# Optimization experiments

Measured on AMD Instinct MI355X. Metric: run time of the kernel, lower is better.

Reference implementation:

```python
import jax, jax.numpy as jnp
import numpy as np

NEG_INF = -1e9  # stands in for the eye(W)*sys.maxsize self-mask on the row axis


def setup_inputs() -> dict:
    key = jax.random.key(0)
    ks = jax.random.split(key, 8)
    B, C, S = 8, 512, 128
    C8 = C // 8
    sc = 0.02
    x = jax.random.normal(ks[0], (B, C, S, S), dtype=jnp.float32)
    Wq = jax.random.normal(ks[1], (C8, C), dtype=jnp.float32) * sc
    bq = jnp.zeros((C8,), dtype=jnp.float32)
    Wk = jax.random.normal(ks[2], (C8, C), dtype=jnp.float32) * sc
    bk = jnp.zeros((C8,), dtype=jnp.float32)
    Wv = jax.random.normal(ks[3], (C, C), dtype=jnp.float32) * sc
    bv = jnp.zeros((C,), dtype=jnp.float32)
    gamma = jnp.ones((1,), dtype=jnp.float32) * 0.5  # source inits to 0; nonzero so path is exercised
    return {"x": x, "Wq": Wq, "bq": bq, "Wk": Wk, "bk": bk, "Wv": Wv, "bv": bv, "gamma": gamma}


def reference(x, Wq, bq, Wk, bk, Wv, bv, gamma):
    # x: (B, C, W, H) with W == H == S (required by the eye-mask view in the source)
    B, C, S, _ = x.shape
    # 1x1 convs = per-pixel linear projections
    q = jnp.einsum('oc,bcwh->bowh', Wq, x) + bq[None, :, None, None]  # (B,C8,S,S)
    k = jnp.einsum('oc,bcwh->bowh', Wk, x) + bk[None, :, None, None]
    v = jnp.einsum('oc,bcwh->bowh', Wv, x) + bv[None, :, None, None]  # (B,C,S,S)

    # column ('h'-fixed) attention along W, self position masked out
    e_col = jnp.einsum('bcwh,bcuh->bwhu', q, k)  # (B,W,H,W)
    self_mask = jnp.eye(S, dtype=bool)  # w == u
    e_col = jnp.where(self_mask[None, :, None, :], NEG_INF, e_col)
    # row ('w'-fixed) attention along H
    e_row = jnp.einsum('bcwh,bcwu->bwhu', q, k)  # (B,W,H,H)

    att = jax.nn.softmax(jnp.concatenate([e_col, e_row], axis=-1), axis=-1)  # (B,W,H,2S)
    a_col = att[..., :S]   # weights over w'
    a_row = att[..., S:]   # weights over h'

    out = (jnp.einsum('bwhu,bcuh->bcwh', a_col, v)
           + jnp.einsum('bwhu,bcwu->bcwh', a_row, v))  # (B,C,S,S)
    return gamma[0] * out + x
```

## Files before the change

kernel.cpp:

```cpp
#include <hip/hip_runtime.h>
#include <hip/hip_bf16.h>


#define S 128
#define SS 16384
#define C 512
#define C8 64
#define NEG_BIG -1000000000.0f

using short8 = __attribute__((ext_vector_type(8))) short;
using f32x4  = __attribute__((ext_vector_type(4))) float;

#define GPTR(p) ((const __attribute__((address_space(1))) void*)(p))
#define LPTR(p) ((__attribute__((address_space(3))) void*)(p))

__device__ __forceinline__ unsigned short f2b(float f){
  union { float f; unsigned u; } v; v.f = f;
  unsigned r = (v.u + 0x7fffu + ((v.u >> 16) & 1u)) >> 16;
  return (unsigned short)r;
}
__device__ __forceinline__ float b2f(unsigned short h){
  union { unsigned u; float f; } v; v.u = ((unsigned)h) << 16;
  return v.f;
}

__global__ __launch_bounds__(256) void k_pack_w(
    const float* __restrict__ Wq, const float* __restrict__ Wk,
    const float* __restrict__ Wv, unsigned short* __restrict__ wall){
  int i = blockIdx.x * 256 + threadIdx.x;
  if (i >= 640 * C) return;
  int co = i >> 9, ci = i & (C - 1);
  float v;
  if (co < 64)        v = Wq[co * C + ci];
  else if (co < 128)  v = Wk[(co - 64) * C + ci];
  else                v = Wv[(co - 128) * C + ci];
  wall[i] = f2b(v);
}

__global__ __launch_bounds__(256) void k_xp(
    const float* __restrict__ x, unsigned short* __restrict__ xp){
  __shared__ unsigned short T[128 * 130] __attribute__((aligned(16)));
  int blk = blockIdx.x;
  int ct = blk & 3; int bw = blk >> 2;
  int w = bw & 127; int b = bw >> 7;
  int tid = threadIdx.x;
  int ci0 = ct * 128;
  const float* xb = x + ((size_t)(b * C + ci0) * S + w) * S;
  #pragma unroll
  for (int p = 0; p < 16; ++p){
    int idx = p * 256 + tid;
    int cc = idx >> 5;
    int h4 = (idx & 31) * 4;
    float4 v = *(const float4*)(xb + (size_t)cc * SS + h4);
    unsigned* d = (unsigned*)&T[cc * 130 + h4];
    d[0] = (unsigned)f2b(v.x) | ((unsigned)f2b(v.y) << 16);
    d[1] = (unsigned)f2b(v.z) | ((unsigned)f2b(v.w) << 16);
  }
  __syncthreads();
  unsigned short* xpb = xp + (size_t)(b * S + w) * S * C + ci0;
  #pragma unroll
  for (int p = 0; p < 8; ++p){
    int idx = p * 256 + tid;
    int h  = idx >> 4;
    int ch = (idx & 15) * 8;
    unsigned short tmp[8] __attribute__((aligned(16)));
    #pragma unroll
    for (int j = 0; j < 8; ++j) tmp[j] = T[(ch + j) * 130 + h];
    *(uint4*)(xpb + (size_t)h * C + ch) = *(uint4*)tmp;
  }
}

__global__ __launch_bounds__(256) void k_qkv(
    const unsigned short* __restrict__ xp, const unsigned short* __restrict__ wall,
    const float* __restrict__ bq, const float* __restrict__ bk,
    const float* __restrict__ bv,
    unsigned short* __restrict__ qp, unsigned short* __restrict__ kp,
    unsigned short* __restrict__ vb){
  __shared__ unsigned short sm[17408] __attribute__((aligned(16)));
  unsigned short* Al = sm;
  unsigned short* Bl = sm + 8192;
  unsigned short* Dl = sm;
  int blk = blockIdx.x;
  int pxsub = blk & 7; int t = blk >> 3;
  int cot = t % 5; int pxg = t / 5;
  int pxt = pxg * 8 + pxsub;
  int w = pxt & 127, b = pxt >> 7;
  int tid = threadIdx.x, lane = tid & 63, wid = tid >> 6;
  int qd = lane >> 4, ln = lane & 15;
  const unsigned short* asrc0 = wall + (size_t)cot * 128 * C;
  const unsigned short* bsrc0 = xp + (size_t)pxt * 128 * C;
  f32x4 acc[4][4];
  #pragma unroll
  for (int i = 0; i < 4; ++i)
    #pragma unroll
    for (int j = 0; j < 4; ++j) acc[i][j] = (f32x4){0.f, 0.f, 0.f, 0.f};

  for (int kw = 0; kw < 8; ++kw){
    __syncthreads();
    const unsigned short* asrc = asrc0 + kw * 64;
    const unsigned short* bsrc = bsrc0 + kw * 64;
    #pragma unroll
    for (int p = 0; p < 4; ++p){
      int gi = p * 256 + tid;
      int row = gi >> 3, kc = (gi & 7) * 8;
      __builtin_amdgcn_global_load_lds(GPTR(asrc + (size_t)row * C + kc),
                                       LPTR((char*)Al + gi * 16), 16, 0, 0);
      __builtin_amdgcn_global_load_lds(GPTR(bsrc + (size_t)row * C + kc),
                                       LPTR((char*)Bl + gi * 16), 16, 0, 0);
    }
    __syncthreads();
    #pragma unroll
    for (int ks = 0; ks < 2; ++ks){
      int ko = ks * 32 + qd * 8;
      short8 af[4], bfr[4];
      #pragma unroll
      for (int i = 0; i < 4; ++i)
        af[i] = *(const short8*)&Al[(((wid & 1) * 4 + i) * 16 + ln) * 64 + ko];
      #pragma unroll
      for (int j = 0; j < 4; ++j)
        bfr[j] = *(const short8*)&Bl[(((wid >> 1) * 4 + j) * 16 + ln) * 64 + ko];
      #pragma unroll
      for (int i = 0; i < 4; ++i)
        #pragma unroll
        for (int j = 0; j < 4; ++j)
          acc[i][j] = __builtin_amdgcn_mfma_f32_16x16x32_bf16(af[i], bfr[j], acc[i][j], 0, 0, 0);
    }
  }
  __syncthreads();
  float bias_[4][4];
  #pragma unroll
  for (int i = 0; i < 4; ++i){
    int co_l0 = ((wid & 1) * 4 + i) * 16 + qd * 4;
    #pragma unroll
    for (int r = 0; r < 4; ++r){
      int co_l = co_l0 + r;
      bias_[i][r] = (cot == 0) ? (co_l < 64 ? bq[co_l] : bk[co_l - 64])
                               : bv[(cot - 1) * 128 + co_l];
    }
  }
  #pragma unroll
  for (int i = 0; i < 4; ++i){
    int co_l0 = ((wid & 1) * 4 + i) * 16 + qd * 4;
    #pragma unroll
    for (int j = 0; j < 4; ++j){
      int pxl = ((wid >> 1) * 4 + j) * 16 + ln;
      #pragma unroll
      for (int r = 0; r < 4; ++r)
        Dl[(co_l0 + r) * 136 + pxl] = f2b(acc[i][j][r] + bias_[i][r]);
    }
  }
  __syncthreads();
  if (cot == 0){
    unsigned short* qb = qp + (size_t)(b * S + w) * S * C8;
    unsigned short* kb = kp + (size_t)(b * S + w) * S * C8;
    #pragma unroll
    for (int p = 0; p < 4; ++p){
      int idx = p * 256 + tid;
      int cch = idx & 7, hh = idx >> 3;
      unsigned short tq[8] __attribute__((aligned(16)));
      unsigned short tk[8] __attribute__((aligned(16)));
      #pragma unroll
      for (int jj = 0; jj < 8; ++jj){
        tq[jj] = Dl[(cch * 8 + jj) * 136 + hh];
        tk[jj] = Dl[(64 + cch * 8 + jj) * 136 + hh];
      }
      *(uint4*)(qb + (size_t)hh * C8 + cch * 8) = *(uint4*)tq;
      *(uint4*)(kb + (size_t)hh * C8 + cch * 8) = *(uint4*)tk;
    }
  } else {
    unsigned short* vbb = vb + ((size_t)(b * C + (cot - 1) * 128) * S + w) * S;
    #pragma unroll
    for (int p = 0; p < 8; ++p){
      int idx = p * 256 + tid;
      int c_l = idx >> 4, hc = (idx & 15) * 8;
      uint4 v = *(const uint4*)&Dl[c_l * 136 + hc];
      *(uint4*)(vbb + (size_t)c_l * SS + hc) = v;
    }
  }
}

__global__ __launch_bounds__(256) void k_tv(
    const unsigned short* __restrict__ vb, unsigned short* __restrict__ vt){
  __shared__ unsigned short T[128 * 130] __attribute__((aligned(16)));
  int bc = blockIdx.x;
  const unsigned short* src = vb + (size_t)bc * SS;
  unsigned short* dst = vt + (size_t)bc * SS;
  int tid = threadIdx.x;
  #pragma unroll
  for (int p = 0; p < 8; ++p){
    int idx = p * 256 + tid;
    int wv = idx >> 4, ch = (idx & 15) * 8;
    uint4 v = *(const uint4*)(src + wv * S + ch);
    unsigned* d = (unsigned*)&T[wv * 130 + ch];
    d[0] = v.x; d[1] = v.y; d[2] = v.z; d[3] = v.w;
  }
  __syncthreads();
  #pragma unroll
  for (int p = 0; p < 8; ++p){
    int idx = p * 256 + tid;
    int h = idx >> 4, ch = (idx & 15) * 8;
    unsigned short tmp[8] __attribute__((aligned(16)));
    #pragma unroll
    for (int j = 0; j < 8; ++j) tmp[j] = T[(ch + j) * 130 + h];
    *(uint4*)(dst + h * S + ch) = *(uint4*)tmp;
  }
}

__global__ __launch_bounds__(256) void k_ecol(
    const unsigned short* __restrict__ qp, const unsigned short* __restrict__ kp,
    unsigned short* __restrict__ eca){
  __shared__ unsigned short Aq[128 * 72] __attribute__((aligned(16)));
  __shared__ unsigned short Bk[128 * 72] __attribute__((aligned(16)));
  int blk = blockIdx.x; int h = blk & 127, b = blk >> 7;
  int tid = threadIdx.x, lane = tid & 63, wid = tid >> 6;
  int qd = lane >> 4, ln = lane & 15;
  #pragma unroll
  for (int p = 0; p < 4; ++p){
    int idx = p * 256 + tid;
    int row = idx >> 3, ch = (idx & 7) * 8;
    *(uint4*)&Aq[row * 72 + ch] = *(const uint4*)(qp + ((size_t)(b * S + row) * S + h) * C8 + ch);
    *(uint4*)&Bk[row * 72 + ch] = *(const uint4*)(kp + ((size_t)(b * S + row) * S + h) * C8 + ch);
  }
  __syncthreads();
  f32x4 acc[4][4];
  #pragma unroll
  for (int i = 0; i < 4; ++i)
    #pragma unroll
    for (int j = 0; j < 4; ++j) acc[i][j] = (f32x4){0.f, 0.f, 0.f, 0.f};
  #pragma unroll
  for (int ks = 0; ks < 2; ++ks){
    int ko = ks * 32 + qd * 8;
    short8 af[4], bfr[4];
    #pragma unroll
    for (int i = 0; i < 4; ++i)
      af[i] = *(const short8*)&Aq[(((wid & 1) * 4 + i) * 16 + ln) * 72 + ko];
    #pragma unroll
    for (int j = 0; j < 4; ++j)
      bfr[j] = *(const short8*)&Bk[(((wid >> 1) * 4 + j) * 16 + ln) * 72 + ko];
    #pragma unroll
    for (int i = 0; i < 4; ++i)
      #pragma unroll
      for (int j = 0; j < 4; ++j)
        acc[i][j] = __builtin_amdgcn_mfma_f32_16x16x32_bf16(af[i], bfr[j], acc[i][j], 0, 0, 0);
  }
  #pragma unroll
  for (int i = 0; i < 4; ++i){
    int w0 = ((wid & 1) * 4 + i) * 16 + qd * 4;
    #pragma unroll
    for (int j = 0; j < 4; ++j){
      int ug = ((wid >> 1) * 4 + j) * 16 + ln;
      #pragma unroll
      for (int r = 0; r < 4; ++r){
        int wg = w0 + r;
        float val = acc[i][j][r];
        if (wg == ug) val = NEG_BIG;
        eca[((size_t)(b * S + wg) * S + h) * S + ug] = f2b(val);
      }
    }
  }
}

__global__ __launch_bounds__(256) void k_erow_softmax(
    const unsigned short* __restrict__ qp, const unsigned short* __restrict__ kp,
    unsigned short* __restrict__ eca, unsigned short* __restrict__ ar){
  __shared__ char sm[36864] __attribute__((aligned(16)));
  unsigned short* Aq = (unsigned short*)sm;
  unsigned short* Bk = (unsigned short*)(sm + 18432);
  unsigned short* El = (unsigned short*)sm;
  float* redm = (float*)(sm + 34816);
  float* reds = (float*)(sm + 35840);
  int blk = blockIdx.x; int w = blk & 127, b = blk >> 7;
  int tid = threadIdx.x, lane = tid & 63, wid = tid >> 6;
  int qd = lane >> 4, ln = lane & 15;
  size_t tb = (size_t)(b * S + w) * SS;
  {
    const unsigned short* qsrc = qp + (size_t)(b * S + w) * S * C8;
    const unsigned short* ksrc = kp + (size_t)(b * S + w) * S * C8;
    #pragma unroll
    for (int p = 0; p < 4; ++p){
      int idx = p * 256 + tid;
      int row = idx >> 3, ch = (idx & 7) * 8;
      *(uint4*)&Aq[row * 72 + ch] = *(const uint4*)(qsrc + row * C8 + ch);
      *(uint4*)&Bk[row * 72 + ch] = *(const uint4*)(ksrc + row * C8 + ch);
    }
  }
  __syncthreads();
  f32x4 acc[4][4];
  #pragma unroll
  for (int i = 0; i < 4; ++i)
    #pragma unroll
    for (int j = 0; j < 4; ++j) acc[i][j] = (f32x4){0.f, 0.f, 0.f, 0.f};
  #pragma unroll
  for (int ks = 0; ks < 2; ++ks){
    int ko = ks * 32 + qd * 8;
    short8 af[4], bfr[4];
    #pragma unroll
    for (int i = 0; i < 4; ++i)
      af[i] = *(const short8*)&Aq[(((wid & 1) * 4 + i) * 16 + ln) * 72 + ko];
    #pragma unroll
    for (int j = 0; j < 4; ++j)
      bfr[j] = *(const short8*)&Bk[(((wid >> 1) * 4 + j) * 16 + ln) * 72 + ko];
    #pragma unroll
    for (int i = 0; i < 4; ++i)
      #pragma unroll
      for (int j = 0; j < 4; ++j)
        acc[i][j] = __builtin_amdgcn_mfma_f32_16x16x32_bf16(af[i], bfr[j], acc[i][j], 0, 0, 0);
  }
  __syncthreads();
  #pragma unroll
  for (int i = 0; i < 4; ++i){
    int h0 = ((wid & 1) * 4 + i) * 16 + qd * 4;
    #pragma unroll
    for (int j = 0; j < 4; ++j){
      int ul = ((wid >> 1) * 4 + j) * 16 + ln;
      #pragma unroll
      for (int r = 0; r < 4; ++r)
        El[(h0 + r) * 136 + ul] = f2b(acc[i][j][r]);
    }
  }
  __syncthreads();
  int h = tid >> 1, half = tid & 1;
  const uint4* src4 = (half == 0) ? (const uint4*)(eca + tb + (size_t)h * S)
                                  : (const uint4*)&El[h * 136];
  float mx = -3.0e38f;
  #pragma unroll 4
  for (int u = 0; u < 16; ++u){
    uint4 v = src4[u];
    const unsigned short* e = (const unsigned short*)&v;
    #pragma unroll
    for (int jj = 0; jj < 8; ++jj) mx = fmaxf(mx, b2f(e[jj]));
  }
  redm[tid] = mx;
  __syncthreads();
  float m = fmaxf(mx, redm[tid ^ 1]);
  float s = 0.f;
  #pragma unroll 4
  for (int u = 0; u < 16; ++u){
    uint4 v = src4[u];
    const unsigned short* e = (const unsigned short*)&v;
    #pragma unroll
    for (int jj = 0; jj < 8; ++jj) s += __expf(b2f(e[jj]) - m);
  }
  reds[tid] = s;
  __syncthreads();
  float inv = 1.0f / (s + reds[tid ^ 1]);
  uint4* dst4 = (half == 0) ? (uint4*)(eca + tb + (size_t)h * S)
                            : (uint4*)(ar + tb + (size_t)h * S);
  #pragma unroll 4
  for (int u = 0; u < 16; ++u){
    uint4 v = src4[u];
    const unsigned short* e = (const unsigned short*)&v;
    unsigned short o[8] __attribute__((aligned(16)));
    #pragma unroll
    for (int jj = 0; jj < 8; ++jj) o[jj] = f2b(__expf(b2f(e[jj]) - m) * inv);
    dst4[u] = *(uint4*)o;
  }
}

__global__ __launch_bounds__(256) void k_outrow(
    const unsigned short* __restrict__ vb, const unsigned short* __restrict__ ar,
    const float* __restrict__ x, const float* __restrict__ gamma,
    float* __restrict__ out){
  __shared__ unsigned short Av[128 * 72] __attribute__((aligned(16)));
  __shared__ unsigned short Ba[128 * 72] __attribute__((aligned(16)));
  int blk = blockIdx.x;
  int ct = blk & 3; int bw = blk >> 2;
  int w = bw & 127, b = bw >> 7;
  int tid = threadIdx.x, lane = tid & 63, wid = tid >> 6;
  int qd = lane >> 4, ln = lane & 15;
  size_t tb = (size_t)(b * S + w) * SS;
  f32x4 acc[4][4];
  #pragma unroll
  for (int i = 0; i < 4; ++i)
    #pragma unroll
    for (int j = 0; j < 4; ++j) acc[i][j] = (f32x4){0.f, 0.f, 0.f, 0.f};
  for (int kw = 0; kw < 2; ++kw){
    __syncthreads();
    #pragma unroll
    for (int p = 0; p < 4; ++p){
      int idx = p * 256 + tid;
      int row = idx >> 3, ch = (idx & 7) * 8;
      *(uint4*)&Av[row * 72 + ch] =
        *(const uint4*)(vb + ((size_t)(b * C + ct * 128 + row) * S + w) * S + kw * 64 + ch);
      *(uint4*)&Ba[row * 72 + ch] =
        *(const uint4*)(ar + tb + (size_t)row * S + kw * 64 + ch);
    }
    __syncthreads();
    #pragma unroll
    for (int ks = 0; ks < 2; ++ks){
      int ko = ks * 32 + qd * 8;
      short8 af[4], bfr[4];
      #pragma unroll
      for (int i = 0; i < 4; ++i)
        af[i] = *(const short8*)&Av[(((wid & 1) * 4 + i) * 16 + ln) * 72 + ko];
      #pragma unroll
      for (int j = 0; j < 4; ++j)
        bfr[j] = *(const short8*)&Ba[(((wid >> 1) * 4 + j) * 16 + ln) * 72 + ko];
      #pragma unroll
      for (int i = 0; i < 4; ++i)
        #pragma unroll
        for (int j = 0; j < 4; ++j)
          acc[i][j] = __builtin_amdgcn_mfma_f32_16x16x32_bf16(af[i], bfr[j], acc[i][j], 0, 0, 0);
    }
  }
  float g = gamma[0];
  #pragma unroll
  for (int i = 0; i < 4; ++i){
    int c0 = ((wid & 1) * 4 + i) * 16 + qd * 4;
    #pragma unroll
    for (int j = 0; j < 4; ++j){
      int hl = ((wid >> 1) * 4 + j) * 16 + ln;
      #pragma unroll
      for (int r = 0; r < 4; ++r){
        int cg = ct * 128 + c0 + r;
        size_t o = ((size_t)(b * C + cg) * S + w) * S + hl;
        out[o] = g * acc[i][j][r] + x[o];
      }
    }
  }
}

__global__ __launch_bounds__(256) void k_outcol(
    const unsigned short* __restrict__ vt, const unsigned short* __restrict__ eca,
    unsigned short* __restrict__ oct){
  __shared__ unsigned short Av[128 * 72] __attribute__((aligned(16)));
  __shared__ unsigned short Ba[128 * 72] __attribute__((aligned(16)));
  int blk = blockIdx.x;
  int ct = blk & 3; int bh = blk >> 2;
  int h = bh & 127, b = bh >> 7;
  int tid = threadIdx.x, lane = tid & 63, wid = tid >> 6;
  int qd = lane >> 4, ln = lane & 15;
  f32x4 acc[4][4];
  #pragma unroll
  for (int i = 0; i < 4; ++i)
    #pragma unroll
    for (int j = 0; j < 4; ++j) acc[i][j] = (f32x4){0.f, 0.f, 0.f, 0.f};
  for (int kw = 0; kw < 2; ++kw){
    __syncthreads();
    #pragma unroll
    for (int p = 0; p < 4; ++p){
      int idx = p * 256 + tid;
      int row = idx >> 3, ch = (idx & 7) * 8;
      *(uint4*)&Av[row * 72 + ch] =
        *(const uint4*)(vt + ((size_t)(b * C + ct * 128 + row) * S + h) * S + kw * 64 + ch);
      *(uint4*)&Ba[row * 72 + ch] =
        *(const uint4*)(eca + ((size_t)(b * S + row) * S + h) * S + kw * 64 + ch);
    }
    __syncthreads();
    #pragma unroll
    for (int ks = 0; ks < 2; ++ks){
      int ko = ks * 32 + qd * 8;
      short8 af[4], bfr[4];
      #pragma unroll
      for (int i = 0; i < 4; ++i)
        af[i] = *(const short8*)&Av[(((wid & 1) * 4 + i) * 16 + ln) * 72 + ko];
      #pragma unroll
      for (int j = 0; j < 4; ++j)
        bfr[j] = *(const short8*)&Ba[(((wid >> 1) * 4 + j) * 16 + ln) * 72 + ko];
      #pragma unroll
      for (int i = 0; i < 4; ++i)
        #pragma unroll
        for (int j = 0; j < 4; ++j)
          acc[i][j] = __builtin_amdgcn_mfma_f32_16x16x32_bf16(af[i], bfr[j], acc[i][j], 0, 0, 0);
    }
  }
  #pragma unroll
  for (int i = 0; i < 4; ++i){
    int c0 = ((wid & 1) * 4 + i) * 16 + qd * 4;
    #pragma unroll
    for (int j = 0; j < 4; ++j){
      int wl = ((wid >> 1) * 4 + j) * 16 + ln;
      #pragma unroll
      for (int r = 0; r < 4; ++r){
        int cg = ct * 128 + c0 + r;
        oct[((size_t)(b * S + h) * C + cg) * S + wl] = f2b(acc[i][j][r]);
      }
    }
  }
}

__global__ __launch_bounds__(256) void k_final(
    const unsigned short* __restrict__ oct, const float* __restrict__ gamma,
    float* __restrict__ out){
  __shared__ unsigned short T[128 * 130] __attribute__((aligned(16)));
  int blk = blockIdx.x;
  int c = blk & 511, b = blk >> 9;
  int tid = threadIdx.x;
  float g = gamma[0];
  #pragma unroll
  for (int p = 0; p < 8; ++p){
    int idx = p * 256 + tid;
    int hh = idx >> 4, ch = (idx & 15) * 8;
    uint4 v = *(const uint4*)(oct + ((size_t)(b * S + hh) * C + c) * S + ch);
    unsigned* d = (unsigned*)&T[hh * 130 + ch];
    d[0] = v.x; d[1] = v.y; d[2] = v.z; d[3] = v.w;
  }
  __syncthreads();
  #pragma unroll
  for (int p = 0; p < 8; ++p){
    int idx = p * 256 + tid;
    int wv = idx >> 4, hch = (idx & 15) * 8;
    size_t o = ((size_t)(b * C + c) * S + wv) * S + hch;
    float4 o0 = *(float4*)(out + o);
    float4 o1 = *(float4*)(out + o + 4);
    o0.x += g * b2f(T[(hch + 0) * 130 + wv]);
    o0.y += g * b2f(T[(hch + 1) * 130 + wv]);
    o0.z += g * b2f(T[(hch + 2) * 130 + wv]);
    o0.w += g * b2f(T[(hch + 3) * 130 + wv]);
    o1.x += g * b2f(T[(hch + 4) * 130 + wv]);
    o1.y += g * b2f(T[(hch + 5) * 130 + wv]);
    o1.z += g * b2f(T[(hch + 6) * 130 + wv]);
    o1.w += g * b2f(T[(hch + 7) * 130 + wv]);
    *(float4*)(out + o) = o0;
    *(float4*)(out + o + 4) = o1;
  }
}

extern "C" void kernel_launch(void* const* d_in, const int* in_sizes, int n_in,
                              void* d_out, int out_size, void* d_ws, size_t ws_size,
                              hipStream_t stream){
  const float* x     = (const float*)d_in[0];
  const float* Wq    = (const float*)d_in[1];
  const float* bq    = (const float*)d_in[2];
  const float* Wk    = (const float*)d_in[3];
  const float* bk    = (const float*)d_in[4];
  const float* Wv    = (const float*)d_in[5];
  const float* bv    = (const float*)d_in[6];
  const float* gamma = (const float*)d_in[7];
  float* out = (float*)d_out;
  char* ws = (char*)d_ws;

  const size_t OFF_WALL = 0;
  const size_t OFF_XP   = 1ull << 20;
  const size_t OFF_QP   = OFF_XP  + 134217728ull;
  const size_t OFF_KP   = OFF_QP  + 16777216ull;
  const size_t OFF_VB   = OFF_KP  + 16777216ull;
  const size_t OFF_VT   = OFF_VB  + 134217728ull;
  const size_t OFF_ECA  = OFF_VT  + 134217728ull;
  const size_t OFF_AR   = OFF_ECA + 33554432ull;
  const size_t OFF_OCT  = OFF_XP;
  const size_t NEED     = OFF_AR + 33554432ull;
  if (ws_size < NEED) return;

  unsigned short* wall = (unsigned short*)(ws + OFF_WALL);
  unsigned short* xp   = (unsigned short*)(ws + OFF_XP);
  unsigned short* qp   = (unsigned short*)(ws + OFF_QP);
  unsigned short* kp   = (unsigned short*)(ws + OFF_KP);
  unsigned short* vb   = (unsigned short*)(ws + OFF_VB);
  unsigned short* vt   = (unsigned short*)(ws + OFF_VT);
  unsigned short* eca  = (unsigned short*)(ws + OFF_ECA);
  unsigned short* ar   = (unsigned short*)(ws + OFF_AR);
  unsigned short* oct  = (unsigned short*)(ws + OFF_OCT);

  k_pack_w      <<<1280, 256, 0, stream>>>(Wq, Wk, Wv, wall);
  k_xp          <<<4096, 256, 0, stream>>>(x, xp);
  k_qkv         <<<5120, 256, 0, stream>>>(xp, wall, bq, bk, bv, qp, kp, vb);
  k_tv          <<<4096, 256, 0, stream>>>(vb, vt);
  k_ecol        <<<1024, 256, 0, stream>>>(qp, kp, eca);
  k_erow_softmax<<<1024, 256, 0, stream>>>(qp, kp, eca, ar);
  k_outrow      <<<4096, 256, 0, stream>>>(vb, ar, x, gamma, out);
  k_outcol      <<<4096, 256, 0, stream>>>(vt, eca, oct);
  k_final       <<<4096, 256, 0, stream>>>(oct, gamma, out);
}
```

Before: 1.099 ms.

## Swizzle QKV GEMM LDS tiles and stage row output as bf16 for final fused epilogue

The QKV projection GEMM now stores its 16-byte chunks into LDS with an XOR swizzle keyed by row. The MFMA fragment loads use the matching swizzle, which is meant to spread lanes reading the same k-offset across different banks. The row-attention output kernel now writes a bf16 intermediate into the freed vt buffer, and runs after the column kernel. k_final then combines row and column results with x in one pass, replacing the old read of x, fp32 write, and later read-modify-write of out. This cuts fp32 output traffic, but the row contribution is now rounded to bf16 before it is added.

```diff
diff --git a/kernel.cpp b/kernel.cpp
--- a/kernel.cpp
+++ b/kernel.cpp
@@ -102,7 +102,8 @@
     #pragma unroll
     for (int p = 0; p < 4; ++p){
       int gi = p * 256 + tid;
-      int row = gi >> 3, kc = (gi & 7) * 8;
+      int row = gi >> 3, cc = gi & 7;
+      int kc = (cc ^ (row & 7)) * 8;
       __builtin_amdgcn_global_load_lds(GPTR(asrc + (size_t)row * C + kc),
                                        LPTR((char*)Al + gi * 16), 16, 0, 0);
       __builtin_amdgcn_global_load_lds(GPTR(bsrc + (size_t)row * C + kc),
@@ -111,14 +112,14 @@
     __syncthreads();
     #pragma unroll
     for (int ks = 0; ks < 2; ++ks){
-      int ko = ks * 32 + qd * 8;
+      int ch8 = (((ks * 4 + qd) ^ (ln & 7)) * 8);
       short8 af[4], bfr[4];
       #pragma unroll
       for (int i = 0; i < 4; ++i)
-        af[i] = *(const short8*)&Al[(((wid & 1) * 4 + i) * 16 + ln) * 64 + ko];
+        af[i] = *(const short8*)&Al[(((wid & 1) * 4 + i) * 16 + ln) * 64 + ch8];
       #pragma unroll
       for (int j = 0; j < 4; ++j)
-        bfr[j] = *(const short8*)&Bl[(((wid >> 1) * 4 + j) * 16 + ln) * 64 + ko];
+        bfr[j] = *(const short8*)&Bl[(((wid >> 1) * 4 + j) * 16 + ln) * 64 + ch8];
       #pragma unroll
       for (int i = 0; i < 4; ++i)
         #pragma unroll
@@ -359,8 +360,7 @@
 
 __global__ __launch_bounds__(256) void k_outrow(
     const unsigned short* __restrict__ vb, const unsigned short* __restrict__ ar,
-    const float* __restrict__ x, const float* __restrict__ gamma,
-    float* __restrict__ out){
+    unsigned short* __restrict__ orw){
   __shared__ unsigned short Av[128 * 72] __attribute__((aligned(16)));
   __shared__ unsigned short Ba[128 * 72] __attribute__((aligned(16)));
   int blk = blockIdx.x;
@@ -403,7 +403,6 @@
           acc[i][j] = __builtin_amdgcn_mfma_f32_16x16x32_bf16(af[i], bfr[j], acc[i][j], 0, 0, 0);
     }
   }
-  float g = gamma[0];
   #pragma unroll
   for (int i = 0; i < 4; ++i){
     int c0 = ((wid & 1) * 4 + i) * 16 + qd * 4;
@@ -413,8 +412,7 @@
       #pragma unroll
       for (int r = 0; r < 4; ++r){
         int cg = ct * 128 + c0 + r;
-        size_t o = ((size_t)(b * C + cg) * S + w) * S + hl;
-        out[o] = g * acc[i][j][r] + x[o];
+        orw[((size_t)(b * C + cg) * S + w) * S + hl] = f2b(acc[i][j][r]);
       }
     }
   }
@@ -480,7 +478,8 @@
 }
 
 __global__ __launch_bounds__(256) void k_final(
-    const unsigned short* __restrict__ oct, const float* __restrict__ gamma,
+    const unsigned short* __restrict__ oct, const unsigned short* __restrict__ orw,
+    const float* __restrict__ x, const float* __restrict__ gamma,
     float* __restrict__ out){
   __shared__ unsigned short T[128 * 130] __attribute__((aligned(16)));
   int blk = blockIdx.x;
@@ -501,16 +500,19 @@
     int idx = p * 256 + tid;
     int wv = idx >> 4, hch = (idx & 15) * 8;
     size_t o = ((size_t)(b * C + c) * S + wv) * S + hch;
-    float4 o0 = *(float4*)(out + o);
-    float4 o1 = *(float4*)(out + o + 4);
-    o0.x += g * b2f(T[(hch + 0) * 130 + wv]);
-    o0.y += g * b2f(T[(hch + 1) * 130 + wv]);
-    o0.z += g * b2f(T[(hch + 2) * 130 + wv]);
-    o0.w += g * b2f(T[(hch + 3) * 130 + wv]);
-    o1.x += g * b2f(T[(hch + 4) * 130 + wv]);
-    o1.y += g * b2f(T[(hch + 5) * 130 + wv]);
-    o1.z += g * b2f(T[(hch + 6) * 130 + wv]);
-    o1.w += g * b2f(T[(hch + 7) * 130 + wv]);
+    uint4 rv = *(const uint4*)(orw + o);
+    const unsigned short* rr = (const unsigned short*)&rv;
+    float4 x0 = *(const float4*)(x + o);
+    float4 x1 = *(const float4*)(x + o + 4);
+    float4 o0, o1;
+    o0.x = g * (b2f(rr[0]) + b2f(T[(hch + 0) * 130 + wv])) + x0.x;
+    o0.y = g * (b2f(rr[1]) + b2f(T[(hch + 1) * 130 + wv])) + x0.y;
+    o0.z = g * (b2f(rr[2]) + b2f(T[(hch + 2) * 130 + wv])) + x0.z;
+    o0.w = g * (b2f(rr[3]) + b2f(T[(hch + 3) * 130 + wv])) + x0.w;
+    o1.x = g * (b2f(rr[4]) + b2f(T[(hch + 4) * 130 + wv])) + x1.x;
+    o1.y = g * (b2f(rr[5]) + b2f(T[(hch + 5) * 130 + wv])) + x1.y;
+    o1.z = g * (b2f(rr[6]) + b2f(T[(hch + 6) * 130 + wv])) + x1.z;
+    o1.w = g * (b2f(rr[7]) + b2f(T[(hch + 7) * 130 + wv])) + x1.w;
     *(float4*)(out + o) = o0;
     *(float4*)(out + o + 4) = o1;
   }
@@ -539,6 +541,7 @@
   const size_t OFF_ECA  = OFF_VT  + 134217728ull;
   const size_t OFF_AR   = OFF_ECA + 33554432ull;
   const size_t OFF_OCT  = OFF_XP;
+  const size_t OFF_ORW  = OFF_VT;
   const size_t NEED     = OFF_AR + 33554432ull;
   if (ws_size < NEED) return;
 
@@ -551,6 +554,7 @@
   unsigned short* eca  = (unsigned short*)(ws + OFF_ECA);
   unsigned short* ar   = (unsigned short*)(ws + OFF_AR);
   unsigned short* oct  = (unsigned short*)(ws + OFF_OCT);
+  unsigned short* orw  = (unsigned short*)(ws + OFF_ORW);
 
   k_pack_w      <<<1280, 256, 0, stream>>>(Wq, Wk, Wv, wall);
   k_xp          <<<4096, 256, 0, stream>>>(x, xp);
@@ -558,7 +562,7 @@
   k_tv          <<<4096, 256, 0, stream>>>(vb, vt);
   k_ecol        <<<1024, 256, 0, stream>>>(qp, kp, eca);
   k_erow_softmax<<<1024, 256, 0, stream>>>(qp, kp, eca, ar);
-  k_outrow      <<<4096, 256, 0, stream>>>(vb, ar, x, gamma, out);
   k_outcol      <<<4096, 256, 0, stream>>>(vt, eca, oct);
-  k_final       <<<4096, 256, 0, stream>>>(oct, gamma, out);
-}
+  k_outrow      <<<4096, 256, 0, stream>>>(vb, ar, orw);
+  k_final       <<<4096, 256, 0, stream>>>(oct, orw, x, gamma, out);
+}
```

Result: faster. 1.026 ms (-6.7%).
